# Kernel tuning notes

Measured on AMD Instinct MI355X. Metric: run time of the kernel, lower is better.

## Reference

```python
import jax, jax.numpy as jnp
import numpy as np

B, S, HID = 1, 2048, 2048   # batch, block_size, hidden_dim
H, D = 16, 128              # num_heads, head_dim
WORLD_SIZE = 4
LOCAL_BLOCK_IDX = 3         # last rank: all kv blocks are causally visible


def setup_inputs() -> dict:
    key = jax.random.key(0)
    ks = jax.random.split(key, 5)
    w = lambda k: jax.random.normal(k, (H * D, HID), dtype=jnp.float32) * 0.02
    return {
        "hidden_states": jax.random.normal(ks[0], (B, S, HID), dtype=jnp.float32),
        "q_w": w(ks[1]), "q_b": jnp.zeros((H * D,), jnp.float32),
        "k_w": w(ks[2]), "k_b": jnp.zeros((H * D,), jnp.float32),
        "v_w": w(ks[3]), "v_b": jnp.zeros((H * D,), jnp.float32),
        "o_w": jax.random.normal(ks[4], (HID, H * D), dtype=jnp.float32) * 0.02,
        "o_b": jnp.zeros((HID,), jnp.float32),
        "world_size": WORLD_SIZE,
        "local_block_idx": LOCAL_BLOCK_IDX,
    }


def reference(hidden_states, q_w, q_b, k_w, k_b, v_w, v_b, o_w, o_b,
              world_size, local_block_idx):
    Bsz, Sq, _ = hidden_states.shape

    def proj(w, b):  # (B,S,HID) -> (B,H,S,D)
        return (hidden_states @ w.T + b).reshape(Bsz, Sq, H, D).transpose(0, 2, 1, 3)

    q, k, v = proj(q_w, q_b), proj(k_w, k_b), proj(v_w, v_b)
    scale = D ** -0.5

    # ring_send_recv is a local copy, so K/V are identical every ring step;
    # only the causal masking differs (triu mask on the diagonal block step).
    scores_base = jnp.einsum('bhqd,bhkd->bhqk', q, k) * scale
    tri = jnp.triu(jnp.ones((Sq, Sq), bool), k=1)
    scores_diag = jnp.where(tri, -jnp.inf, scores_base)

    out = jnp.zeros((Bsz, H, Sq, D), hidden_states.dtype)
    mx = jnp.full((Bsz, H, Sq, 1), -jnp.inf, hidden_states.dtype)
    se = jnp.zeros((Bsz, H, Sq, 1), hidden_states.dtype)

    for step in range(world_size):  # small fixed ring loop
        kv_idx = (local_block_idx - step) % world_size
        scores = scores_diag if kv_idx == local_block_idx else scores_base
        # OnlineSoftmax.update (faithful, including block-wise normalization)
        bm = scores.max(axis=-1, keepdims=True)
        nm = jnp.maximum(mx, bm)
        old_s = jnp.exp(mx - nm)
        new_s = jnp.exp(bm - nm)
        be = jnp.exp(scores - bm)
        bs = be.sum(axis=-1, keepdims=True)
        se = se * old_s + bs * new_s
        aw = be / (bs + 1e-8)
        bo = jnp.einsum('bhqk,bhkd->bhqd', aw, v)
        out = out * old_s + bo * new_s
        mx = nm

    out = out / (se + 1e-8)  # OnlineSoftmax.finalize
    out = out.transpose(0, 2, 1, 3).reshape(Bsz, Sq, H * D)
    return out @ o_w.T + o_b
```

## Files before the change

### kernel.cpp

```cpp
#include <hip/hip_runtime.h>
#include <hip/hip_bf16.h>
#include <stdint.h>
#include <stddef.h>


typedef __attribute__((ext_vector_type(8))) short bf16x8;
typedef __attribute__((ext_vector_type(4))) float f32x4;

#define MFMA_BF16(a, b, c) __builtin_amdgcn_mfma_f32_16x16x32_bf16((a), (b), (c), 0, 0, 0)

__device__ __forceinline__ void load16_lds(const void* g, void* l) {
  __builtin_amdgcn_global_load_lds((const __attribute__((address_space(1))) void*)g,
                                   (__attribute__((address_space(3))) void*)l,
                                   16, 0, 0);
}

__device__ __forceinline__ unsigned short f2bf(float x) {
  union { __hip_bfloat16 b; unsigned short u; } cv;
  cv.b = __float2bfloat16(x);
  return cv.u;
}

__global__ __launch_bounds__(256) void cvt_all(
    const float4* __restrict__ s0, const float4* __restrict__ s1,
    const float4* __restrict__ s2, const float4* __restrict__ s3,
    const float4* __restrict__ s4,
    ushort4* __restrict__ d0, ushort4* __restrict__ d1,
    ushort4* __restrict__ d2, ushort4* __restrict__ d3,
    ushort4* __restrict__ d4) {
  const int seg = blockIdx.x >> 12;
  const int i = ((blockIdx.x & 4095) << 8) + threadIdx.x;
  const float4* s = seg == 0 ? s0 : seg == 1 ? s1 : seg == 2 ? s2 : seg == 3 ? s3 : s4;
  ushort4* d = seg == 0 ? d0 : seg == 1 ? d1 : seg == 2 ? d2 : seg == 3 ? d3 : d4;
  float4 v = s[i];
  ushort4 o;
  o.x = f2bf(v.x); o.y = f2bf(v.y); o.z = f2bf(v.z); o.w = f2bf(v.w);
  d[i] = o;
}

__global__ __launch_bounds__(512, 2) void gemm_qkv(
    const unsigned short* __restrict__ A, const unsigned short* __restrict__ Bt,
    const float* __restrict__ qb, const float* __restrict__ kb,
    const float* __restrict__ vb,
    unsigned short* __restrict__ Qo, unsigned short* __restrict__ Ko,
    unsigned short* __restrict__ Vt) {
  __shared__ __align__(16) unsigned short sA[2][2][128 * 64];
  __shared__ __align__(16) unsigned short sB[2][2][128 * 64];
  const int tid = threadIdx.x;
  const int wave = tid >> 6, lane = tid & 63;
  const int quad = lane >> 4, l16 = lane & 15;
  const int wr = wave >> 2, wc = wave & 3;
  const int m0 = blockIdx.y << 8, n0 = blockIdx.x << 8;

  f32x4 acc[8][4] = {};
  bf16x8 af[8], bf01[2], bf23[2];

  const int sc_ = (lane & 7) ^ (lane >> 3);
  const int srow16 = 2 * (lane >> 3) + (sc_ >> 2);
  const int scol8 = (sc_ & 3) * 8;

  auto stageA = [&](int kt_, int ks_) {
    unsigned short* dst = &sA[kt_ & 1][ks_][wave * 512];
    const unsigned short* src =
        A + (size_t)(m0 + wave * 16 + srow16) * 2048 + kt_ * 64 + ks_ * 32 + scol8;
#pragma unroll
    for (int rr = 0; rr < 2; rr++)
      load16_lds(src + (size_t)rr * 128 * 2048, dst + rr * 4096);
  };
  auto stageB = [&](int kt_, int ks_) {
    unsigned short* dst = &sB[kt_ & 1][ks_][wave * 512];
    const unsigned short* src =
        Bt + (size_t)(n0 + wave * 16 + srow16) * 2048 + kt_ * 64 + ks_ * 32 + scol8;
#pragma unroll
    for (int rr = 0; rr < 2; rr++)
      load16_lds(src + (size_t)rr * 128 * 2048, dst + rr * 4096);
  };

  const int hl = l16 >> 1;
  const int pos8 = ((((l16 & 1) << 2) + quad) ^ hl) << 3;
  const int aoff = (wr * 64 + hl) * 64 + pos8;
  const int boff = (wc * 32 + hl) * 64 + pos8;

#define PHASE(KS, NB, BF, READ_A, STAGE_STMT, VM_STMT)                         \
  {                                                                            \
    const unsigned short* sAp = &sA[kt & 1][KS][aoff];                         \
    const unsigned short* sBp = &sB[kt & 1][KS][boff];                         \
    if (READ_A) {                                                              \
      _Pragma("unroll") for (int mi = 0; mi < 8; mi++)                         \
          af[mi] = *(const bf16x8*)(sAp + mi * 512);                           \
    }                                                                          \
    _Pragma("unroll") for (int j = 0; j < 2; j++)                              \
        BF[j] = *(const bf16x8*)(sBp + (NB + j) * 512);                        \
    STAGE_STMT;                                                                \
    __builtin_amdgcn_s_barrier();                                              \
    asm volatile("s_waitcnt lgkmcnt(0)" ::: "memory");                         \
    __builtin_amdgcn_s_setprio(1);                                             \
    _Pragma("unroll") for (int mi = 0; mi < 8; mi++) {                         \
      acc[mi][NB] = MFMA_BF16(af[mi], BF[0], acc[mi][NB]);                     \
      acc[mi][NB + 1] = MFMA_BF16(af[mi], BF[1], acc[mi][NB + 1]);             \
    }                                                                          \
    __builtin_amdgcn_s_setprio(0);                                             \
    VM_STMT;                                                                   \
    __builtin_amdgcn_s_barrier();                                              \
  }

  stageA(0, 0); stageB(0, 0); stageA(0, 1); stageB(0, 1);
  asm volatile("s_waitcnt vmcnt(4)" ::: "memory");
  __builtin_amdgcn_s_barrier();

  for (int kt = 0; kt < 32; kt++) {
    const bool pf = (kt < 31);
    PHASE(0, 0, bf01, true,  { if (pf) stageA(kt + 1, 0); }, {});
    PHASE(0, 2, bf23, false, { if (pf) stageB(kt + 1, 0); },
          {
            asm volatile("s_waitcnt vmcnt(4)" ::: "memory");
            if (kt == 31)
              asm volatile("s_waitcnt vmcnt(0)" ::: "memory");
          });
    PHASE(1, 0, bf01, true,  { if (pf) stageA(kt + 1, 1); }, {});
    PHASE(1, 2, bf23, false, { if (pf) stageB(kt + 1, 1); },
          { asm volatile("s_waitcnt vmcnt(4)" ::: "memory"); });
  }
#undef PHASE
  asm volatile("s_waitcnt vmcnt(0)" ::: "memory");

  const float qscale = 0.088388347648318447f * 1.4426950408889634f;
#pragma unroll
  for (int mi = 0; mi < 8; mi++) {
    const int row = m0 + wr * 128 + mi * 16 + quad * 4;
#pragma unroll
    for (int ni = 0; ni < 4; ni++) {
      const int col = n0 + wc * 64 + ni * 16 + l16;
#pragma unroll
      for (int r = 0; r < 4; r++) {
        const float v = acc[mi][ni][r];
        const int rr = row + r;
        if (col < 2048) {
          const int hh = col >> 7, d = col & 127;
          Qo[((size_t)hh * 2048 + rr) * 128 + d] = f2bf((v + qb[col]) * qscale);
        } else if (col < 4096) {
          const int f = col - 2048;
          const int hh = f >> 7, d = f & 127;
          Ko[((size_t)hh * 2048 + rr) * 128 + d] = f2bf(v + kb[f]);
        } else {
          const int f = col - 4096;
          const int hh = f >> 7, d = f & 127;
          Vt[((size_t)hh * 128 + d) * 2048 + rr] = f2bf(v + vb[f]);
        }
      }
    }
  }
}

__global__ __launch_bounds__(256, 2) void attn_fwd(
    const unsigned short* __restrict__ Q, const unsigned short* __restrict__ K,
    const unsigned short* __restrict__ V,
    unsigned short* __restrict__ O,
    const int* __restrict__ wsp) {
  const int qt = blockIdx.y, h = blockIdx.x;
  const int tid = threadIdx.x;
  const int wave = tid >> 6, lane = tid & 63;
  const int quad = lane >> 4, l16 = lane & 15;

  __shared__ __align__(16) unsigned short sK0[64 * 128];
  __shared__ __align__(16) unsigned short sK1[64 * 128];
  __shared__ __align__(16) unsigned short sV0[128 * 64];
  __shared__ __align__(16) unsigned short sV1[128 * 64];
  __shared__ __align__(16) unsigned short sP[4][16 * 64];

  const unsigned short* Qh = Q + (size_t)h * 2048 * 128;
  const unsigned short* Kh = K + (size_t)h * 2048 * 128;
  const unsigned short* Vh = V + (size_t)h * 128 * 2048;
  unsigned short* sPw = sP[wave];

  for (int c = wave; c < 16; c += 4) {
    const int rowc = lane >> 4;
    const int row = c * 4 + rowc;
    const int blk = (lane & 15) ^ (row & 15);
    load16_lds(Qh + (size_t)(qt * 64 + row) * 128 + blk * 8, &sK0[c * 512]);
  }
  __syncthreads();

  bf16x8 qf[4];
#pragma unroll
  for (int ds = 0; ds < 4; ds++)
    qf[ds] = *(const bf16x8*)&sK0[(wave * 16 + l16) * 128 + (((ds * 4 + quad) ^ l16) << 3)];
  __syncthreads();

  float m1 = -3.0e38f, l1 = 0.f, m2 = -3.0e38f, l2 = 0.f;
  f32x4 o1[8], o2[8];
#pragma unroll
  for (int j = 0; j < 8; j++) { o1[j] = f32x4{0.f, 0.f, 0.f, 0.f}; o2[j] = f32x4{0.f, 0.f, 0.f, 0.f}; }

  auto stageKV = [&](int kt, unsigned short* kDst, unsigned short* vDst) {
    const int k0 = kt << 6;
    for (int c = wave; c < 16; c += 4) {
      {
        const int rowc = lane >> 4;
        const int row = c * 4 + rowc;
        const int blk = (lane & 15) ^ (row & 15);
        load16_lds(Kh + (size_t)(k0 + row) * 128 + blk * 8, &kDst[c * 512]);
      }
      {
        const int rowc = lane >> 3;
        const int row = c * 8 + rowc;
        const int blk = (lane & 7) ^ (rowc & 7);
        load16_lds(Vh + (size_t)row * 2048 + k0 + blk * 8, &vDst[c * 512]);
      }
    }
  };

  auto softmax_update = [&](float& m, float& l, f32x4 (&o)[8],
                            const f32x4 (&stt)[4], bool masked, int k0) {
    const int qg = qt * 64 + wave * 16 + l16;
    float t[4][4];
    float mx = -3.0e38f;
#pragma unroll
    for (int ni = 0; ni < 4; ni++)
#pragma unroll
      for (int r = 0; r < 4; r++) {
        float v = stt[ni][r];
        if (masked && (k0 + ni * 16 + quad * 4 + r > qg)) v = -3.0e38f;
        t[ni][r] = v;
        mx = fmaxf(mx, v);
      }
    mx = fmaxf(mx, __shfl_xor(mx, 16));
    mx = fmaxf(mx, __shfl_xor(mx, 32));
    const float mn = fmaxf(m, mx);
    const float al = exp2f(m - mn);
    float rs = 0.f;
#pragma unroll
    for (int ni = 0; ni < 4; ni++) {
      union { unsigned short u[4]; uint2 v; } pk;
#pragma unroll
      for (int r = 0; r < 4; r++) {
        const float p = exp2f(t[ni][r] - mn);
        rs += p;
        pk.u[r] = f2bf(p);
      }
      const int off =
          l16 * 64 + (((ni * 2 + (quad >> 1)) ^ (l16 & 7)) << 3) + ((quad & 1) << 2);
      *(uint2*)&sPw[off] = pk.v;
    }
    rs += __shfl_xor(rs, 16);
    rs += __shfl_xor(rs, 32);
    const bool grew = !__all(mn == m);
    l = l * al + rs;
    m = mn;
    if (grew) {
#pragma unroll
      for (int r = 0; r < 4; r++) {
        const int src = (lane & 48) + quad * 4 + r;
        const float ab = __shfl(al, src);
#pragma unroll
        for (int j = 0; j < 8; j++) o[j][r] *= ab;
      }
    }
  };

  auto pv = [&](f32x4 (&o)[8], const unsigned short* vBuf) {
#pragma unroll
    for (int ks = 0; ks < 2; ks++) {
      const int cs = (((ks * 4 + quad) ^ (l16 & 7)) << 3);
      const bf16x8 pf = *(const bf16x8*)&sPw[l16 * 64 + cs];
#pragma unroll
      for (int j = 0; j < 8; j++) {
        const bf16x8 vf = *(const bf16x8*)&vBuf[(j * 16 + l16) * 64 + cs];
        o[j] = MFMA_BF16(pf, vf, o[j]);
      }
    }
  };

  auto compute_tile = [&](int kt, const unsigned short* kBuf,
                          const unsigned short* vBuf) {
    const int k0 = kt << 6;
    f32x4 st[4];
#pragma unroll
    for (int ni = 0; ni < 4; ni++) st[ni] = f32x4{0.f, 0.f, 0.f, 0.f};
#pragma unroll
    for (int ds = 0; ds < 4; ds++) {
#pragma unroll
      for (int ni = 0; ni < 4; ni++) {
        const bf16x8 kf =
            *(const bf16x8*)&kBuf[(ni * 16 + l16) * 128 + (((ds * 4 + quad) ^ l16) << 3)];
        st[ni] = MFMA_BF16(kf, qf[ds], st[ni]);
      }
    }

    if (kt == qt) {
      m1 = m2; l1 = l2;
#pragma unroll
      for (int j = 0; j < 8; j++) o1[j] = o2[j];
      softmax_update(m1, l1, o1, st, true, k0);
      pv(o1, vBuf);
    }
    softmax_update(m2, l2, o2, st, false, k0);
    pv(o2, vBuf);
  };

  stageKV(0, sK0, sV0);
  for (int kt2 = 0; kt2 < 32; kt2 += 2) {
    __syncthreads();
    if (kt2 + 1 < 32) stageKV(kt2 + 1, sK1, sV1);
    compute_tile(kt2, sK0, sV0);
    __syncthreads();
    if (kt2 + 2 < 32) stageKV(kt2 + 2, sK0, sV0);
    compute_tile(kt2 + 1, sK1, sV1);
  }

  const float fws = (float)(wsp[0] - 1);
  const float a = exp2f(m1 - m2);
  const float se = l1 * a + fws * l2;
  const float inv = 1.0f / (se + 1e-8f);
  const float f1 = (a / (l1 + 1e-8f)) * inv;
  const float f2 = (fws / (l2 + 1e-8f)) * inv;
#pragma unroll
  for (int r = 0; r < 4; r++) {
    const int src = (lane & 48) + quad * 4 + r;
    const float f1b = __shfl(f1, src);
    const float f2b = __shfl(f2, src);
    const int row = qt * 64 + wave * 16 + quad * 4 + r;
#pragma unroll
    for (int j = 0; j < 8; j++) {
      const float ov = o1[j][r] * f1b + o2[j][r] * f2b;
      O[(size_t)row * 2048 + h * 128 + j * 16 + l16] = f2bf(ov);
    }
  }
}

__global__ __launch_bounds__(256) void gemm_o(
    const unsigned short* __restrict__ A, const unsigned short* __restrict__ Bt,
    const float* __restrict__ ob, float* __restrict__ Cout) {
  __shared__ __align__(16) unsigned short sA[64 * 128];
  __shared__ __align__(16) unsigned short sB[128 * 128];
  const int tid = threadIdx.x;
  const int wave = tid >> 6, lane = tid & 63;
  const int quad = lane >> 4, l16 = lane & 15;
  const int wm = wave >> 1, wn = wave & 1;
  const int m0 = blockIdx.y << 6, n0 = blockIdx.x << 7;

  f32x4 acc[2][4] = {};

  for (int k0 = 0; k0 < 2048; k0 += 128) {
    __syncthreads();
#pragma unroll
    for (int t = 0; t < 4; t++) {
      const int i = t * 4 + wave;
      const int idx = i * 64 + lane;
      const int row = idx >> 4;
      const int c = (idx & 15) ^ (row & 15);
      load16_lds(A + (size_t)(m0 + row) * 2048 + k0 + c * 8, &sA[i * 512]);
    }
#pragma unroll
    for (int t = 0; t < 8; t++) {
      const int i = t * 4 + wave;
      const int idx = i * 64 + lane;
      const int row = idx >> 4;
      const int c = (idx & 15) ^ (row & 15);
      load16_lds(Bt + (size_t)(n0 + row) * 2048 + k0 + c * 8, &sB[i * 512]);
    }
    __syncthreads();
#pragma unroll
    for (int ks = 0; ks < 4; ks++) {
      const int cs = ((ks * 4 + quad) ^ l16) << 3;
      bf16x8 af[2], bfr[4];
#pragma unroll
      for (int i = 0; i < 2; i++)
        af[i] = *(const bf16x8*)&sA[(wm * 32 + i * 16 + l16) * 128 + cs];
#pragma unroll
      for (int i = 0; i < 4; i++)
        bfr[i] = *(const bf16x8*)&sB[(wn * 64 + i * 16 + l16) * 128 + cs];
#pragma unroll
      for (int mi = 0; mi < 2; mi++)
#pragma unroll
        for (int ni = 0; ni < 4; ni++)
          acc[mi][ni] = MFMA_BF16(af[mi], bfr[ni], acc[mi][ni]);
    }
  }

#pragma unroll
  for (int mi = 0; mi < 2; mi++) {
    const int row = m0 + wm * 32 + mi * 16 + quad * 4;
#pragma unroll
    for (int ni = 0; ni < 4; ni++) {
      const int col = n0 + wn * 64 + ni * 16 + l16;
#pragma unroll
      for (int r = 0; r < 4; r++) {
        Cout[(size_t)(row + r) * 2048 + col] = acc[mi][ni][r] + ob[col];
      }
    }
  }
}

extern "C" void kernel_launch(void* const* d_in, const int* in_sizes, int n_in,
                              void* d_out, int out_size, void* d_ws, size_t ws_size,
                              hipStream_t stream) {
  (void)in_sizes; (void)n_in; (void)out_size; (void)ws_size;
  const float* hs = (const float*)d_in[0];
  const float* qw = (const float*)d_in[1];
  const float* qb = (const float*)d_in[2];
  const float* kw = (const float*)d_in[3];
  const float* kb = (const float*)d_in[4];
  const float* vw = (const float*)d_in[5];
  const float* vb = (const float*)d_in[6];
  const float* ow = (const float*)d_in[7];
  const float* ob = (const float*)d_in[8];
  const int* wsz = (const int*)d_in[9];

  char* w = (char*)d_ws;
  unsigned short* hsb  = (unsigned short*)(w + 0);
  unsigned short* wqkv = (unsigned short*)(w + 8388608);
  unsigned short* owb  = (unsigned short*)(w + 33554432);
  unsigned short* Qb_  = (unsigned short*)(w + 41943040);
  unsigned short* Kb_  = (unsigned short*)(w + 50331648);
  unsigned short* Vtb  = (unsigned short*)(w + 58720256);
  unsigned short* atb  = (unsigned short*)(w + 67108864);

  cvt_all<<<20480, 256, 0, stream>>>(
      (const float4*)hs, (const float4*)qw, (const float4*)kw, (const float4*)vw,
      (const float4*)ow,
      (ushort4*)hsb, (ushort4*)wqkv, (ushort4*)(wqkv + 4194304),
      (ushort4*)(wqkv + 8388608), (ushort4*)owb);

  gemm_qkv<<<dim3(24, 8), 512, 0, stream>>>(hsb, wqkv, qb, kb, vb, Qb_, Kb_, Vtb);
  attn_fwd<<<dim3(16, 32), 256, 0, stream>>>(Qb_, Kb_, Vtb, atb, wsz);
  gemm_o<<<dim3(16, 32), 256, 0, stream>>>(atb, owb, ob, (float*)d_out);
}
```

Measured before the change: 310.1 us.

## Software-pipeline QK of the next tile ahead of softmax and PV

Restructures the attention main loop so the QK^T MFMAs for tile kt+1 are issued before the softmax and PV of tile kt. K and V staging are split and staggered: K is prefetched two tiles ahead and V one tile ahead. This leaves a single barrier per iteration, and the Q staging now reuses a V buffer so the separate barrier after loading Q goes away. MFMA sections are wrapped in s_setprio to favour matrix issue. The extra in-flight score registers (stn) add register pressure under launch_bounds(256,2), which could cause spills.

```diff
diff --git a/kernel.cpp b/kernel.cpp
--- a/kernel.cpp
+++ b/kernel.cpp
@@ -162,10 +162,8 @@
   const int wave = tid >> 6, lane = tid & 63;
   const int quad = lane >> 4, l16 = lane & 15;
 
-  __shared__ __align__(16) unsigned short sK0[64 * 128];
-  __shared__ __align__(16) unsigned short sK1[64 * 128];
-  __shared__ __align__(16) unsigned short sV0[128 * 64];
-  __shared__ __align__(16) unsigned short sV1[128 * 64];
+  __shared__ __align__(16) unsigned short sK[2][64 * 128];
+  __shared__ __align__(16) unsigned short sV[2][128 * 64];
   __shared__ __align__(16) unsigned short sP[4][16 * 64];
 
   const unsigned short* Qh = Q + (size_t)h * 2048 * 128;
@@ -173,41 +171,58 @@
   const unsigned short* Vh = V + (size_t)h * 128 * 2048;
   unsigned short* sPw = sP[wave];
 
+  auto stageK = [&](int kt, int b) {
+    const int k0 = kt << 6;
+    for (int c = wave; c < 16; c += 4) {
+      const int rowc = lane >> 4;
+      const int row = c * 4 + rowc;
+      const int blk = (lane & 15) ^ (row & 15);
+      load16_lds(Kh + (size_t)(k0 + row) * 128 + blk * 8, &sK[b][c * 512]);
+    }
+  };
+  auto stageV = [&](int kt, int b) {
+    const int k0 = kt << 6;
+    for (int c = wave; c < 16; c += 4) {
+      const int rowc = lane >> 3;
+      const int row = c * 8 + rowc;
+      const int blk = (lane & 7) ^ (rowc & 7);
+      load16_lds(Vh + (size_t)row * 2048 + k0 + blk * 8, &sV[b][c * 512]);
+    }
+  };
+
   for (int c = wave; c < 16; c += 4) {
     const int rowc = lane >> 4;
     const int row = c * 4 + rowc;
     const int blk = (lane & 15) ^ (row & 15);
-    load16_lds(Qh + (size_t)(qt * 64 + row) * 128 + blk * 8, &sK0[c * 512]);
-  }
+    load16_lds(Qh + (size_t)(qt * 64 + row) * 128 + blk * 8, &sV[1][c * 512]);
+  }
+  stageK(0, 0); stageV(0, 0); stageK(1, 1);
   __syncthreads();
 
   bf16x8 qf[4];
 #pragma unroll
   for (int ds = 0; ds < 4; ds++)
-    qf[ds] = *(const bf16x8*)&sK0[(wave * 16 + l16) * 128 + (((ds * 4 + quad) ^ l16) << 3)];
-  __syncthreads();
+    qf[ds] = *(const bf16x8*)&sV[1][(wave * 16 + l16) * 128 + (((ds * 4 + quad) ^ l16) << 3)];
 
   float m1 = -3.0e38f, l1 = 0.f, m2 = -3.0e38f, l2 = 0.f;
   f32x4 o1[8], o2[8];
 #pragma unroll
   for (int j = 0; j < 8; j++) { o1[j] = f32x4{0.f, 0.f, 0.f, 0.f}; o2[j] = f32x4{0.f, 0.f, 0.f, 0.f}; }
 
-  auto stageKV = [&](int kt, unsigned short* kDst, unsigned short* vDst) {
-    const int k0 = kt << 6;
-    for (int c = wave; c < 16; c += 4) {
-      {
-        const int rowc = lane >> 4;
-        const int row = c * 4 + rowc;
-        const int blk = (lane & 15) ^ (row & 15);
-        load16_lds(Kh + (size_t)(k0 + row) * 128 + blk * 8, &kDst[c * 512]);
-      }
-      {
-        const int rowc = lane >> 3;
-        const int row = c * 8 + rowc;
-        const int blk = (lane & 7) ^ (rowc & 7);
-        load16_lds(Vh + (size_t)row * 2048 + k0 + blk * 8, &vDst[c * 512]);
-      }
-    }
+  auto qk = [&](int b, f32x4 (&st)[4]) {
+#pragma unroll
+    for (int ni = 0; ni < 4; ni++) st[ni] = f32x4{0.f, 0.f, 0.f, 0.f};
+    __builtin_amdgcn_s_setprio(1);
+#pragma unroll
+    for (int ds = 0; ds < 4; ds++) {
+#pragma unroll
+      for (int ni = 0; ni < 4; ni++) {
+        const bf16x8 kf =
+            *(const bf16x8*)&sK[b][(ni * 16 + l16) * 128 + (((ds * 4 + quad) ^ l16) << 3)];
+        st[ni] = MFMA_BF16(kf, qf[ds], st[ni]);
+      }
+    }
+    __builtin_amdgcn_s_setprio(0);
   };
 
   auto softmax_update = [&](float& m, float& l, f32x4 (&o)[8],
@@ -259,6 +274,7 @@
   };
 
   auto pv = [&](f32x4 (&o)[8], const unsigned short* vBuf) {
+    __builtin_amdgcn_s_setprio(1);
 #pragma unroll
     for (int ks = 0; ks < 2; ks++) {
       const int cs = (((ks * 4 + quad) ^ (l16 & 7)) << 3);
@@ -269,43 +285,29 @@
         o[j] = MFMA_BF16(pf, vf, o[j]);
       }
     }
-  };
-
-  auto compute_tile = [&](int kt, const unsigned short* kBuf,
-                          const unsigned short* vBuf) {
+    __builtin_amdgcn_s_setprio(0);
+  };
+
+  f32x4 stc[4], stn[4];
+  qk(0, stc);
+
+  for (int kt = 0; kt < 32; kt++) {
+    __syncthreads();
+    if (kt + 2 < 32) stageK(kt + 2, kt & 1);
+    if (kt + 1 < 32) stageV(kt + 1, (kt + 1) & 1);
+    if (kt + 1 < 32) qk((kt + 1) & 1, stn);
     const int k0 = kt << 6;
-    f32x4 st[4];
-#pragma unroll
-    for (int ni = 0; ni < 4; ni++) st[ni] = f32x4{0.f, 0.f, 0.f, 0.f};
-#pragma unroll
-    for (int ds = 0; ds < 4; ds++) {
-#pragma unroll
-      for (int ni = 0; ni < 4; ni++) {
-        const bf16x8 kf =
-            *(const bf16x8*)&kBuf[(ni * 16 + l16) * 128 + (((ds * 4 + quad) ^ l16) << 3)];
-        st[ni] = MFMA_BF16(kf, qf[ds], st[ni]);
-      }
-    }
-
     if (kt == qt) {
       m1 = m2; l1 = l2;
 #pragma unroll
       for (int j = 0; j < 8; j++) o1[j] = o2[j];
-      softmax_update(m1, l1, o1, st, true, k0);
-      pv(o1, vBuf);
-    }
-    softmax_update(m2, l2, o2, st, false, k0);
-    pv(o2, vBuf);
-  };
-
-  stageKV(0, sK0, sV0);
-  for (int kt2 = 0; kt2 < 32; kt2 += 2) {
-    __syncthreads();
-    if (kt2 + 1 < 32) stageKV(kt2 + 1, sK1, sV1);
-    compute_tile(kt2, sK0, sV0);
-    __syncthreads();
-    if (kt2 + 2 < 32) stageKV(kt2 + 2, sK0, sV0);
-    compute_tile(kt2 + 1, sK1, sV1);
+      softmax_update(m1, l1, o1, stc, true, k0);
+      pv(o1, &sV[kt & 1][0]);
+    }
+    softmax_update(m2, l2, o2, stc, false, k0);
+    pv(o2, &sV[kt & 1][0]);
+#pragma unroll
+    for (int ni = 0; ni < 4; ni++) stc[ni] = stn[ni];
   }
 
   const float fws = (float)(wsp[0] - 1);
```

Result: no change. 311.6 us (+0.5%).
